# Optimization experiments

Hardware: AMD Instinct MI355X
Metric: run time of the kernel (lower is better)

The kernel has to match this reference:

```python
import jax, jax.numpy as jnp
import numpy as np

N = 40000      # nodes
E = 640000     # edges
G = 2048       # graphs
D = 128        # emb_dim
T = 10         # num_tasks
L = 5          # layers
ATOM_VOCAB = 64
BOND_VOCAB = 8
BN_EPS = 1e-5


def _bn(x, g, b, m, v):
    # inference-mode BatchNorm1d with running stats
    return (x - m) * jax.lax.rsqrt(v + BN_EPS) * g + b


def setup_inputs() -> dict:
    key = jax.random.key(0)
    ks = jax.random.split(key, 24)
    inp = {
        "x_atom": jax.random.randint(ks[0], (N, 9), 0, ATOM_VOCAB),
        "edge_index": jax.random.randint(ks[1], (2, E), 0, N),
        "edge_attr": jax.random.randint(ks[2], (E, 3), 0, BOND_VOCAB),
        "batch": jnp.sort(jax.random.randint(ks[3], (N,), 0, G)),
        # embedding tables
        "atom_emb": jax.random.normal(ks[4], (9, ATOM_VOCAB, D)) * 0.1,
        "bond_emb": jax.random.normal(ks[5], (L, 3, BOND_VOCAB, D)) * 0.1,
        # per-layer GIN params (stacked over L)
        "eps": jnp.zeros((L,)),
        "W1": jax.random.normal(ks[6], (L, D, 2 * D)) * 0.05,
        "b1": jnp.zeros((L, 2 * D)),
        "g1": jnp.ones((L, 2 * D)),
        "bt1": jnp.zeros((L, 2 * D)),
        "m1": jax.random.normal(ks[7], (L, 2 * D)) * 0.1,
        "v1": jax.random.uniform(ks[8], (L, 2 * D), minval=0.5, maxval=1.5),
        "W2": jax.random.normal(ks[9], (L, 2 * D, D)) * 0.05,
        "b2": jnp.zeros((L, D)),
        # outer BatchNorm per layer
        "gO": jnp.ones((L, D)),
        "btO": jnp.zeros((L, D)),
        "mO": jax.random.normal(ks[10], (L, D)) * 0.1,
        "vO": jax.random.uniform(ks[11], (L, D), minval=0.5, maxval=1.5),
        # prediction head
        "Wp": jax.random.normal(ks[12], (D, T)) * 0.05,
        "bp": jnp.zeros((T,)),
    }
    return inp


def reference(x_atom, edge_index, edge_attr, batch, atom_emb, bond_emb, eps,
              W1, b1, g1, bt1, m1, v1, W2, b2, gO, btO, mO, vO, Wp, bp):
    src, dst = edge_index[0], edge_index[1]
    # AtomEncoder: sum of per-feature embeddings -> [N, D]
    x = atom_emb[jnp.arange(9)[None, :], x_atom].sum(axis=1)
    feat3 = jnp.arange(3)[None, :]
    for i in range(L):
        # BondEncoder for this layer -> [E, D]
        e = bond_emb[i][feat3, edge_attr].sum(axis=1)
        # message: relu(x_j + edge_emb); aggregate: scatter-add at dst
        msg = jax.nn.relu(x[src] + e)
        agg = jax.ops.segment_sum(msg, dst, num_segments=N)
        h = (1.0 + eps[i]) * x + agg
        # MLP: Linear -> BN -> ReLU -> Linear
        h = jax.nn.relu(_bn(h @ W1[i] + b1[i], g1[i], bt1[i], m1[i], v1[i]))
        h = h @ W2[i] + b2[i]
        # outer BN; ReLU after all but last layer (dropout = identity in eval)
        x = _bn(h, gO[i], btO[i], mO[i], vO[i])
        if i < L - 1:
            x = jax.nn.relu(x)
    # global mean pool over graphs
    sums = jax.ops.segment_sum(x, batch, num_segments=G)
    cnt = jax.ops.segment_sum(jnp.ones((N,), x.dtype), batch, num_segments=G)
    pooled = sums / jnp.maximum(cnt, 1.0)[:, None]
    return pooled @ Wp + bp
```

## Files before the change

### kernel.cpp

```cpp
#include <hip/hip_runtime.h>
#include <hip/hip_bf16.h>

#define NN 40000
#define NE 640000
#define NG 2048
#define DD 128
#define NT 10
#define NL 5

typedef __attribute__((ext_vector_type(8))) short short8;
typedef __attribute__((ext_vector_type(4))) float f32x4;
typedef unsigned short ushort_t;

static __device__ __forceinline__ ushort_t f2b(float f) {
    return __bfloat16_as_ushort(__float2bfloat16(f));
}
static __device__ __forceinline__ float b2f(ushort_t u) {
    return __bfloat162float(__ushort_as_bfloat16(u));
}

__global__ void k_atom(const int* __restrict__ xa, const float* __restrict__ emb,
                       ushort_t* __restrict__ x16) {
    int n = blockIdx.x, d = threadIdx.x;
    __shared__ int idx[9];
    if (d < 9) idx[d] = xa[n * 9 + d];
    __syncthreads();
    float s = 0.f;
#pragma unroll
    for (int f = 0; f < 9; ++f) s += emb[(f * 64 + idx[f]) * DD + d];
    x16[n * DD + d] = f2b(s);
}


__global__ void k_hist(const int* __restrict__ ei, int* __restrict__ deg) {
    int e = blockIdx.x * 256 + threadIdx.x;
    atomicAdd(&deg[ei[NE + e]], 1);
}

__global__ void k_scan1(const int* __restrict__ deg, int* __restrict__ off,
                        int* __restrict__ blksum) {
    int b = blockIdx.x, t = threadIdx.x;
    int i = b * 256 + t;
    __shared__ int s[256];
    int v = (i < NN) ? deg[i] : 0;
    s[t] = v;
    __syncthreads();
    for (int d = 1; d < 256; d <<= 1) {
        int add = (t >= d) ? s[t - d] : 0;
        __syncthreads();
        s[t] += add;
        __syncthreads();
    }
    if (i <= NN) off[i] = s[t] - v;
    if (t == 255) blksum[b] = s[255];
}

__global__ void k_scan2(int* __restrict__ blk) {
    int t = threadIdx.x;
    __shared__ int s[256];
    int v = blk[t];
    s[t] = v;
    __syncthreads();
    for (int d = 1; d < 256; d <<= 1) {
        int add = (t >= d) ? s[t - d] : 0;
        __syncthreads();
        s[t] += add;
        __syncthreads();
    }
    blk[256 + t] = s[t] - v;
}

__global__ void k_scan3(int* __restrict__ off, const int* __restrict__ blk) {
    int b = blockIdx.x, t = threadIdx.x;
    int i = b * 256 + t;
    if (i <= NN) off[i] += blk[256 + b];
}

__global__ void k_scatter(const int* __restrict__ ei, const int* __restrict__ ea,
                          const int* __restrict__ off, int* __restrict__ cursor,
                          int2* __restrict__ epack) {
    int e = blockIdx.x * 256 + threadIdx.x;
    int src = ei[e];
    int dst = ei[NE + e];
    int a0 = ea[e * 3 + 0], a1 = ea[e * 3 + 1], a2 = ea[e * 3 + 2];
    int p = off[dst] + atomicAdd(&cursor[dst], 1);
    epack[p] = make_int2(src, a0 | (a1 << 3) | (a2 << 6));
}

__global__ void k_ebsum(const float* __restrict__ bemb, ushort_t* __restrict__ ebsum16) {
    int tid = blockIdx.x * 256 + threadIdx.x;
    int d = tid & 127;
    int c = (tid >> 7) & 511;
    int l = tid >> 16;
    const float* bl = bemb + (size_t)l * 3 * 8 * DD;
    ebsum16[tid] = f2b(bl[(c & 7) * DD + d] + bl[(8 + ((c >> 3) & 7)) * DD + d] +
                       bl[(16 + (c >> 6)) * DD + d]);
}

__global__ void k_prep(const float* __restrict__ W1, const float* __restrict__ W2,
                       ushort_t* __restrict__ W1P, ushort_t* __restrict__ W2P) {
    int tid = blockIdx.x * 256 + threadIdx.x;
    int layer = tid >> 16;
    int r = tid & 65535;
    int half = r >> 15;
    int q = r & 32767;
    int j = q & 7;
    int lane = (q >> 3) & 63;
    if (half == 0) {
        int kk = (q >> 9) & 3;
        int nt = q >> 11;
        int n = nt * 16 + (lane & 15);
        int k = kk * 32 + (lane >> 4) * 8 + j;
        W1P[layer * 32768 + q] = f2b(W1[(layer * DD + k) * 256 + n]);
    } else {
        int kk = (q >> 9) & 7;
        int nt = q >> 12;
        int n = nt * 16 + (lane & 15);
        int k = kk * 32 + (lane >> 4) * 8 + j;
        W2P[layer * 32768 + q] = f2b(W2[(layer * 256 + k) * DD + n]);
    }
}

__global__ void __launch_bounds__(256)
k_gather(const ushort_t* __restrict__ xin, const int* __restrict__ off,
         const int2* __restrict__ epack, const ushort_t* __restrict__ ebsum16,
         const float* __restrict__ eps, int layer, ushort_t* __restrict__ h16) {
    int t = threadIdx.x;
    int lane = t & 63;
    int n = blockIdx.x * 4 + (t >> 6);
    const ushort2* x2 = (const ushort2*)xin;
    const ushort2* eb2 = (const ushort2*)ebsum16;
    ushort2 xv = x2[n * 64 + lane];
    float es = 1.f + eps[layer];
    float ax = es * b2f(xv.x), ay = es * b2f(xv.y);
    int p = off[n], p1 = off[n + 1];

    int2 e0, e1, e2, e3;
    bool have = (p + 4 <= p1);
    if (have) { e0 = epack[p]; e1 = epack[p + 1]; e2 = epack[p + 2]; e3 = epack[p + 3]; }
    while (have) {
        int np = p + 4;
        bool nh = (np + 4 <= p1);
        int2 f0, f1, f2, f3;
        if (nh) { f0 = epack[np]; f1 = epack[np + 1]; f2 = epack[np + 2]; f3 = epack[np + 3]; }
        ushort2 v0 = eb2[e0.y * 64 + lane];
        ushort2 s0 = x2[e0.x * 64 + lane];
        ushort2 v1 = eb2[e1.y * 64 + lane];
        ushort2 s1 = x2[e1.x * 64 + lane];
        ushort2 v2 = eb2[e2.y * 64 + lane];
        ushort2 s2 = x2[e2.x * 64 + lane];
        ushort2 v3 = eb2[e3.y * 64 + lane];
        ushort2 s3 = x2[e3.x * 64 + lane];
        ax += fmaxf(b2f(v0.x) + b2f(s0.x), 0.f) + fmaxf(b2f(v1.x) + b2f(s1.x), 0.f) +
              fmaxf(b2f(v2.x) + b2f(s2.x), 0.f) + fmaxf(b2f(v3.x) + b2f(s3.x), 0.f);
        ay += fmaxf(b2f(v0.y) + b2f(s0.y), 0.f) + fmaxf(b2f(v1.y) + b2f(s1.y), 0.f) +
              fmaxf(b2f(v2.y) + b2f(s2.y), 0.f) + fmaxf(b2f(v3.y) + b2f(s3.y), 0.f);
        p = np;
        e0 = f0; e1 = f1; e2 = f2; e3 = f3;
        have = nh;
    }
    for (; p < p1; ++p) {
        int2 er = epack[p];
        ushort2 ev = eb2[er.y * 64 + lane];
        ushort2 sv = x2[er.x * 64 + lane];
        ax += fmaxf(b2f(ev.x) + b2f(sv.x), 0.f);
        ay += fmaxf(b2f(ev.y) + b2f(sv.y), 0.f);
    }
    ushort2 o;
    o.x = f2b(ax);
    o.y = f2b(ay);
    ((ushort2*)h16)[n * 64 + lane] = o;
}

__global__ void __launch_bounds__(256)
k_mlp_mfma(const ushort_t* __restrict__ h16, const ushort_t* __restrict__ W1P,
           const ushort_t* __restrict__ W2P, const float* __restrict__ b1,
           const float* __restrict__ g1, const float* __restrict__ bt1,
           const float* __restrict__ m1, const float* __restrict__ v1,
           const float* __restrict__ b2_, const float* __restrict__ gO,
           const float* __restrict__ btO, const float* __restrict__ mO,
           const float* __restrict__ vO, int relu, ushort_t* __restrict__ xout) {
    __shared__ ushort_t aS[16 * 136];
    __shared__ ushort_t mid[16 * 264];
    int t = threadIdx.x;
    int wave = t >> 6, lane = t & 63;
    int row0 = blockIdx.x * 16;
    int lrow = lane & 15, quad = lane >> 4;

    {
        int r = t >> 4, c = (t & 15) * 8;
        *(short8*)&aS[r * 136 + c] = *(const short8*)&h16[(row0 + r) * DD + c];
    }
    __syncthreads();

    f32x4 acc1[4];
#pragma unroll
    for (int i = 0; i < 4; ++i) acc1[i] = (f32x4){0.f, 0.f, 0.f, 0.f};
#pragma unroll
    for (int kk = 0; kk < 4; ++kk) {
        short8 af = *(const short8*)&aS[lrow * 136 + kk * 32 + quad * 8];
#pragma unroll
        for (int i = 0; i < 4; ++i) {
            int nt = wave * 4 + i;
            short8 bf = *(const short8*)&W1P[((nt * 4 + kk) * 64 + lane) * 8];
            acc1[i] = __builtin_amdgcn_mfma_f32_16x16x32_bf16(af, bf, acc1[i], 0, 0, 0);
        }
    }
#pragma unroll
    for (int i = 0; i < 4; ++i) {
        int col = (wave * 4 + i) * 16 + lrow;
        float s1 = g1[col] * rsqrtf(v1[col] + 1e-5f);
        float sh = bt1[col] - (m1[col] - b1[col]) * s1;
#pragma unroll
        for (int r = 0; r < 4; ++r) {
            int row = quad * 4 + r;
            float o = acc1[i][r] * s1 + sh;
            mid[row * 264 + col] = f2b(fmaxf(o, 0.f));
        }
    }
    __syncthreads();

    f32x4 acc2[2];
#pragma unroll
    for (int i = 0; i < 2; ++i) acc2[i] = (f32x4){0.f, 0.f, 0.f, 0.f};
#pragma unroll
    for (int kk = 0; kk < 8; ++kk) {
        short8 af = *(const short8*)&mid[lrow * 264 + kk * 32 + quad * 8];
#pragma unroll
        for (int i = 0; i < 2; ++i) {
            int nt = wave * 2 + i;
            short8 bf = *(const short8*)&W2P[((nt * 8 + kk) * 64 + lane) * 8];
            acc2[i] = __builtin_amdgcn_mfma_f32_16x16x32_bf16(af, bf, acc2[i], 0, 0, 0);
        }
    }
#pragma unroll
    for (int i = 0; i < 2; ++i) {
        int col = (wave * 2 + i) * 16 + lrow;
        float s = gO[col] * rsqrtf(vO[col] + 1e-5f);
        float sh = btO[col] - (mO[col] - b2_[col]) * s;
#pragma unroll
        for (int r = 0; r < 4; ++r) {
            int row = quad * 4 + r;
            float o = acc2[i][r] * s + sh;
            if (relu) o = fmaxf(o, 0.f);
            xout[(row0 + row) * DD + col] = f2b(o);
        }
    }
}

__global__ void k_pool(const ushort_t* __restrict__ x16, const int* __restrict__ batch,
                       float* __restrict__ pooled) {
    int g = blockIdx.x, d = threadIdx.x;
    int lo = 0, hi = NN;
    while (lo < hi) { int m = (lo + hi) >> 1; if (batch[m] < g) lo = m + 1; else hi = m; }
    int start = lo;
    hi = NN;
    while (lo < hi) { int m = (lo + hi) >> 1; if (batch[m] < g + 1) lo = m + 1; else hi = m; }
    int end = lo;
    float s = 0.f;
    for (int n = start; n < end; ++n) s += b2f(x16[n * DD + d]);
    float c = fmaxf((float)(end - start), 1.f);
    pooled[g * DD + d] = s / c;
}

__global__ void k_head(const float* __restrict__ pooled, const float* __restrict__ Wp,
                       const float* __restrict__ bp, float* __restrict__ out) {
    int g = blockIdx.x;
    int d = threadIdx.x;
    __shared__ float p[DD];
    p[d] = pooled[g * DD + d];
    __syncthreads();
    if (d < NT) {
        float acc = bp[d];
#pragma unroll 8
        for (int k = 0; k < DD; ++k) acc = fmaf(p[k], Wp[k * NT + d], acc);
        out[g * NT + d] = acc;
    }
}

extern "C" void kernel_launch(void* const* d_in, const int* in_sizes, int n_in,
                              void* d_out, int out_size, void* d_ws, size_t ws_size,
                              hipStream_t stream) {
    const int* x_atom = (const int*)d_in[0];
    const int* edge_index = (const int*)d_in[1];
    const int* edge_attr = (const int*)d_in[2];
    const int* batch = (const int*)d_in[3];
    const float* atom_emb = (const float*)d_in[4];
    const float* bond_emb = (const float*)d_in[5];
    const float* eps = (const float*)d_in[6];
    const float* W1 = (const float*)d_in[7];
    const float* b1 = (const float*)d_in[8];
    const float* g1 = (const float*)d_in[9];
    const float* bt1 = (const float*)d_in[10];
    const float* m1 = (const float*)d_in[11];
    const float* v1 = (const float*)d_in[12];
    const float* W2 = (const float*)d_in[13];
    const float* b2 = (const float*)d_in[14];
    const float* gO = (const float*)d_in[15];
    const float* btO = (const float*)d_in[16];
    const float* mO = (const float*)d_in[17];
    const float* vO = (const float*)d_in[18];
    const float* Wp = (const float*)d_in[19];
    const float* bp = (const float*)d_in[20];

    ushort_t* x16a = (ushort_t*)d_ws;
    ushort_t* x16b = x16a + NN * DD;
    ushort_t* h16 = x16b + NN * DD;
    float* pooled = (float*)(h16 + NN * DD);
    ushort_t* W1P = (ushort_t*)(pooled + NG * DD);
    ushort_t* W2P = W1P + NL * 32768;
    ushort_t* ebsum16 = W2P + NL * 32768;
    int* deg = (int*)(ebsum16 + NL * 65536);
    int* off = deg + NN;
    int* blk = off + 40064;
    int* cursor = blk + 512;
    int2* epack = (int2*)(cursor + NN);

    hipMemsetAsync(deg, 0, (NN + 40064 + 512 + NN) * sizeof(int), stream);

    k_prep<<<NL * 65536 / 256, 256, 0, stream>>>(W1, W2, W1P, W2P);
    k_ebsum<<<NL * 65536 / 256, 256, 0, stream>>>(bond_emb, ebsum16);
    k_atom<<<NN, DD, 0, stream>>>(x_atom, atom_emb, x16a);

    k_hist<<<NE / 256, 256, 0, stream>>>(edge_index, deg);
    k_scan1<<<157, 256, 0, stream>>>(deg, off, blk);
    k_scan2<<<1, 256, 0, stream>>>(blk);
    k_scan3<<<157, 256, 0, stream>>>(off, blk);
    k_scatter<<<NE / 256, 256, 0, stream>>>(edge_index, edge_attr, off, cursor, epack);

    for (int i = 0; i < NL; ++i) {
        ushort_t* xin = (i & 1) ? x16b : x16a;
        ushort_t* xout = (i & 1) ? x16a : x16b;
        k_gather<<<NN / 4, 256, 0, stream>>>(xin, off, epack, ebsum16 + i * 65536,
                                             eps, i, h16);
        k_mlp_mfma<<<NN / 16, 256, 0, stream>>>(
            h16, W1P + (size_t)i * 32768, W2P + (size_t)i * 32768, b1 + i * 256,
            g1 + i * 256, bt1 + i * 256, m1 + i * 256, v1 + i * 256, b2 + i * DD,
            gO + i * DD, btO + i * DD, mO + i * DD, vO + i * DD,
            (i < NL - 1) ? 1 : 0, xout);
    }
    k_pool<<<NG, DD, 0, stream>>>(x16b, batch, pooled);
    k_head<<<NG, DD, 0, stream>>>(pooled, Wp, bp, (float*)d_out);
}
```

Before: 470.6 us.

## Bucket edges before CSR scatter, merge table prep kernels, widen MLP tile

The CSR build now runs in two passes. A bucketing pass groups edges by destination range (512 nodes per bucket) using shared-memory histograms, then a second pass scatters the bucketed edges so the atomics and writes stay local. The weight-packing and bond-embedding-sum kernels are merged into one launch. The MLP kernel now processes 32 rows per block instead of 16, so each B-fragment load is reused across two MFMA row tiles, at the cost of more registers and shared memory. The src field is packed into 16 bits, which works only because N is below 65536.

```diff
diff --git a/kernel.cpp b/kernel.cpp
--- a/kernel.cpp
+++ b/kernel.cpp
@@ -7,6 +7,7 @@
 #define DD 128
 #define NT 10
 #define NL 5
+#define NB 80
 
 typedef __attribute__((ext_vector_type(8))) short short8;
 typedef __attribute__((ext_vector_type(4))) float f32x4;
@@ -76,29 +77,52 @@
     if (i <= NN) off[i] += blk[256 + b];
 }
 
-__global__ void k_scatter(const int* __restrict__ ei, const int* __restrict__ ea,
-                          const int* __restrict__ off, int* __restrict__ cursor,
-                          int2* __restrict__ epack) {
-    int e = blockIdx.x * 256 + threadIdx.x;
-    int src = ei[e];
-    int dst = ei[NE + e];
-    int a0 = ea[e * 3 + 0], a1 = ea[e * 3 + 1], a2 = ea[e * 3 + 2];
+__global__ void __launch_bounds__(256)
+k_bucket(const int* __restrict__ ei, const int* __restrict__ ea,
+         const int* __restrict__ off, int* __restrict__ gbk,
+         int2* __restrict__ ebuf) {
+    __shared__ int hist[NB];
+    __shared__ int sbase[NB];
+    int t = threadIdx.x;
+    int e0 = blockIdx.x * 1024;
+    if (t < NB) hist[t] = 0;
+    __syncthreads();
+    int rank[4], buck[4], rec[4], dstv[4];
+#pragma unroll
+    for (int k = 0; k < 4; ++k) {
+        int e = e0 + k * 256 + t;
+        int src = ei[e];
+        int dst = ei[NE + e];
+        int a0 = ea[e * 3 + 0], a1 = ea[e * 3 + 1], a2 = ea[e * 3 + 2];
+        rec[k] = src | ((a0 | (a1 << 3) | (a2 << 6)) << 16);
+        dstv[k] = dst;
+        int b = dst >> 9;
+        buck[k] = b;
+        rank[k] = atomicAdd(&hist[b], 1);
+    }
+    __syncthreads();
+    if (t < NB) sbase[t] = atomicAdd(&gbk[t], hist[t]);
+    __syncthreads();
+#pragma unroll
+    for (int k = 0; k < 4; ++k) {
+        int b = buck[k];
+        int slot = off[b << 9] + sbase[b] + rank[k];
+        ebuf[slot] = make_int2(rec[k], dstv[k]);
+    }
+}
+
+__global__ void k_scatter2(const int2* __restrict__ ebuf, const int* __restrict__ off,
+                           int* __restrict__ cursor, int2* __restrict__ epack) {
+    int i = blockIdx.x * 256 + threadIdx.x;
+    int2 s = ebuf[i];
+    int dst = s.y;
     int p = off[dst] + atomicAdd(&cursor[dst], 1);
-    epack[p] = make_int2(src, a0 | (a1 << 3) | (a2 << 6));
-}
-
-__global__ void k_ebsum(const float* __restrict__ bemb, ushort_t* __restrict__ ebsum16) {
-    int tid = blockIdx.x * 256 + threadIdx.x;
-    int d = tid & 127;
-    int c = (tid >> 7) & 511;
-    int l = tid >> 16;
-    const float* bl = bemb + (size_t)l * 3 * 8 * DD;
-    ebsum16[tid] = f2b(bl[(c & 7) * DD + d] + bl[(8 + ((c >> 3) & 7)) * DD + d] +
-                       bl[(16 + (c >> 6)) * DD + d]);
-}
-
-__global__ void k_prep(const float* __restrict__ W1, const float* __restrict__ W2,
-                       ushort_t* __restrict__ W1P, ushort_t* __restrict__ W2P) {
+    epack[p] = make_int2(s.x & 0xFFFF, s.x >> 16);
+}
+
+__global__ void k_tables(const float* __restrict__ W1, const float* __restrict__ W2,
+                         const float* __restrict__ bemb, ushort_t* __restrict__ W1P,
+                         ushort_t* __restrict__ W2P, ushort_t* __restrict__ ebsum16) {
     int tid = blockIdx.x * 256 + threadIdx.x;
     int layer = tid >> 16;
     int r = tid & 65535;
@@ -119,6 +143,11 @@
         int k = kk * 32 + (lane >> 4) * 8 + j;
         W2P[layer * 32768 + q] = f2b(W2[(layer * 256 + k) * DD + n]);
     }
+    int d = tid & 127;
+    int c = (tid >> 7) & 511;
+    const float* bl = bemb + (size_t)layer * 3 * 8 * DD;
+    ebsum16[tid] = f2b(bl[(c & 7) * DD + d] + bl[(8 + ((c >> 3) & 7)) * DD + d] +
+                       bl[(16 + (c >> 6)) * DD + d]);
 }
 
 __global__ void __launch_bounds__(256)
@@ -180,30 +209,36 @@
            const float* __restrict__ b2_, const float* __restrict__ gO,
            const float* __restrict__ btO, const float* __restrict__ mO,
            const float* __restrict__ vO, int relu, ushort_t* __restrict__ xout) {
-    __shared__ ushort_t aS[16 * 136];
-    __shared__ ushort_t mid[16 * 264];
+    __shared__ ushort_t aS[32 * 136];
+    __shared__ ushort_t mid[32 * 264];
     int t = threadIdx.x;
     int wave = t >> 6, lane = t & 63;
-    int row0 = blockIdx.x * 16;
+    int row0 = blockIdx.x * 32;
     int lrow = lane & 15, quad = lane >> 4;
 
-    {
-        int r = t >> 4, c = (t & 15) * 8;
+#pragma unroll
+    for (int ps = 0; ps < 2; ++ps) {
+        int idx = ps * 256 + t;
+        int r = idx >> 4, c = (idx & 15) * 8;
         *(short8*)&aS[r * 136 + c] = *(const short8*)&h16[(row0 + r) * DD + c];
     }
     __syncthreads();
 
-    f32x4 acc1[4];
-#pragma unroll
-    for (int i = 0; i < 4; ++i) acc1[i] = (f32x4){0.f, 0.f, 0.f, 0.f};
+    f32x4 acc1[2][4];
+#pragma unroll
+    for (int rt = 0; rt < 2; ++rt)
+#pragma unroll
+        for (int i = 0; i < 4; ++i) acc1[rt][i] = (f32x4){0.f, 0.f, 0.f, 0.f};
 #pragma unroll
     for (int kk = 0; kk < 4; ++kk) {
-        short8 af = *(const short8*)&aS[lrow * 136 + kk * 32 + quad * 8];
+        short8 af0 = *(const short8*)&aS[lrow * 136 + kk * 32 + quad * 8];
+        short8 af1 = *(const short8*)&aS[(16 + lrow) * 136 + kk * 32 + quad * 8];
 #pragma unroll
         for (int i = 0; i < 4; ++i) {
             int nt = wave * 4 + i;
             short8 bf = *(const short8*)&W1P[((nt * 4 + kk) * 64 + lane) * 8];
-            acc1[i] = __builtin_amdgcn_mfma_f32_16x16x32_bf16(af, bf, acc1[i], 0, 0, 0);
+            acc1[0][i] = __builtin_amdgcn_mfma_f32_16x16x32_bf16(af0, bf, acc1[0][i], 0, 0, 0);
+            acc1[1][i] = __builtin_amdgcn_mfma_f32_16x16x32_bf16(af1, bf, acc1[1][i], 0, 0, 0);
         }
     }
 #pragma unroll
@@ -212,25 +247,31 @@
         float s1 = g1[col] * rsqrtf(v1[col] + 1e-5f);
         float sh = bt1[col] - (m1[col] - b1[col]) * s1;
 #pragma unroll
-        for (int r = 0; r < 4; ++r) {
-            int row = quad * 4 + r;
-            float o = acc1[i][r] * s1 + sh;
-            mid[row * 264 + col] = f2b(fmaxf(o, 0.f));
-        }
-    }
-    __syncthreads();
-
-    f32x4 acc2[2];
-#pragma unroll
-    for (int i = 0; i < 2; ++i) acc2[i] = (f32x4){0.f, 0.f, 0.f, 0.f};
+        for (int rt = 0; rt < 2; ++rt)
+#pragma unroll
+            for (int r = 0; r < 4; ++r) {
+                int row = rt * 16 + quad * 4 + r;
+                float o = acc1[rt][i][r] * s1 + sh;
+                mid[row * 264 + col] = f2b(fmaxf(o, 0.f));
+            }
+    }
+    __syncthreads();
+
+    f32x4 acc2[2][2];
+#pragma unroll
+    for (int rt = 0; rt < 2; ++rt)
+#pragma unroll
+        for (int i = 0; i < 2; ++i) acc2[rt][i] = (f32x4){0.f, 0.f, 0.f, 0.f};
 #pragma unroll
     for (int kk = 0; kk < 8; ++kk) {
-        short8 af = *(const short8*)&mid[lrow * 264 + kk * 32 + quad * 8];
+        short8 af0 = *(const short8*)&mid[lrow * 264 + kk * 32 + quad * 8];
+        short8 af1 = *(const short8*)&mid[(16 + lrow) * 264 + kk * 32 + quad * 8];
 #pragma unroll
         for (int i = 0; i < 2; ++i) {
             int nt = wave * 2 + i;
             short8 bf = *(const short8*)&W2P[((nt * 8 + kk) * 64 + lane) * 8];
-            acc2[i] = __builtin_amdgcn_mfma_f32_16x16x32_bf16(af, bf, acc2[i], 0, 0, 0);
+            acc2[0][i] = __builtin_amdgcn_mfma_f32_16x16x32_bf16(af0, bf, acc2[0][i], 0, 0, 0);
+            acc2[1][i] = __builtin_amdgcn_mfma_f32_16x16x32_bf16(af1, bf, acc2[1][i], 0, 0, 0);
         }
     }
 #pragma unroll
@@ -239,12 +280,14 @@
         float s = gO[col] * rsqrtf(vO[col] + 1e-5f);
         float sh = btO[col] - (mO[col] - b2_[col]) * s;
 #pragma unroll
-        for (int r = 0; r < 4; ++r) {
-            int row = quad * 4 + r;
-            float o = acc2[i][r] * s + sh;
-            if (relu) o = fmaxf(o, 0.f);
-            xout[(row0 + row) * DD + col] = f2b(o);
-        }
+        for (int rt = 0; rt < 2; ++rt)
+#pragma unroll
+            for (int r = 0; r < 4; ++r) {
+                int row = rt * 16 + quad * 4 + r;
+                float o = acc2[rt][i][r] * s + sh;
+                if (relu) o = fmaxf(o, 0.f);
+                xout[(row0 + row) * DD + col] = f2b(o);
+            }
     }
 }
 
@@ -314,26 +357,28 @@
     int* off = deg + NN;
     int* blk = off + 40064;
     int* cursor = blk + 512;
-    int2* epack = (int2*)(cursor + NN);
-
-    hipMemsetAsync(deg, 0, (NN + 40064 + 512 + NN) * sizeof(int), stream);
-
-    k_prep<<<NL * 65536 / 256, 256, 0, stream>>>(W1, W2, W1P, W2P);
-    k_ebsum<<<NL * 65536 / 256, 256, 0, stream>>>(bond_emb, ebsum16);
+    int* gbk = cursor + NN;
+    int2* epack = (int2*)(gbk + 128);
+    int2* ebuf = epack + NE;
+
+    hipMemsetAsync(deg, 0, (NN + 40064 + 512 + NN + 128) * sizeof(int), stream);
+
+    k_tables<<<NL * 65536 / 256, 256, 0, stream>>>(W1, W2, bond_emb, W1P, W2P, ebsum16);
     k_atom<<<NN, DD, 0, stream>>>(x_atom, atom_emb, x16a);
 
     k_hist<<<NE / 256, 256, 0, stream>>>(edge_index, deg);
     k_scan1<<<157, 256, 0, stream>>>(deg, off, blk);
     k_scan2<<<1, 256, 0, stream>>>(blk);
     k_scan3<<<157, 256, 0, stream>>>(off, blk);
-    k_scatter<<<NE / 256, 256, 0, stream>>>(edge_index, edge_attr, off, cursor, epack);
+    k_bucket<<<NE / 1024, 256, 0, stream>>>(edge_index, edge_attr, off, gbk, ebuf);
+    k_scatter2<<<NE / 256, 256, 0, stream>>>(ebuf, off, cursor, epack);
 
     for (int i = 0; i < NL; ++i) {
         ushort_t* xin = (i & 1) ? x16b : x16a;
         ushort_t* xout = (i & 1) ? x16a : x16b;
         k_gather<<<NN / 4, 256, 0, stream>>>(xin, off, epack, ebsum16 + i * 65536,
                                              eps, i, h16);
-        k_mlp_mfma<<<NN / 16, 256, 0, stream>>>(
+        k_mlp_mfma<<<NN / 32, 256, 0, stream>>>(
             h16, W1P + (size_t)i * 32768, W2P + (size_t)i * 32768, b1 + i * 256,
             g1 + i * 256, bt1 + i * 256, m1 + i * 256, v1 + i * 256, b2 + i * DD,
             gO + i * DD, btO + i * DD, mO + i * DD, vO + i * DD,
```

After: 435.7 us. 7.4% less time.
